# Optimization experiments

Measured on AMD Instinct MI355X. Metric: run time of the kernel, lower is better.

## Reference

```python
import jax, jax.numpy as jnp
import numpy as np

S, B, D, H, A = 256, 1024, 64, 128, 8  # seq_len, buffer, state_size, hidden, action_size


def _init(key, shape, fan_in):
    bound = 1.0 / np.sqrt(fan_in)
    return jax.random.uniform(key, shape, jnp.float32, -bound, bound)


def setup_inputs() -> dict:
    key = jax.random.key(0)
    ks = jax.random.split(key, 24)
    inp = {"state": jax.random.normal(ks[0], (S, B, D), jnp.float32)}
    # actor / critic MLPs (Linear(D,H) + ReLU + Linear(H,H) + ReLU)
    inp["aw1"] = _init(ks[1], (H, D), D); inp["ab1"] = _init(ks[2], (H,), D)
    inp["aw2"] = _init(ks[3], (H, H), H); inp["ab2"] = _init(ks[4], (H,), H)
    inp["cw1"] = _init(ks[5], (H, D), D); inp["cb1"] = _init(ks[6], (H,), D)
    inp["cw2"] = _init(ks[7], (H, H), H); inp["cb2"] = _init(ks[8], (H,), H)
    # LSTMs (PyTorch layout: W_ih [4H,H], W_hh [4H,H], gate order i,f,g,o)
    inp["a_wih"] = _init(ks[9], (4 * H, H), H); inp["a_whh"] = _init(ks[10], (4 * H, H), H)
    inp["a_bih"] = _init(ks[11], (4 * H,), H); inp["a_bhh"] = _init(ks[12], (4 * H,), H)
    inp["c_wih"] = _init(ks[13], (4 * H, H), H); inp["c_whh"] = _init(ks[14], (4 * H, H), H)
    inp["c_bih"] = _init(ks[15], (4 * H,), H); inp["c_bhh"] = _init(ks[16], (4 * H,), H)
    # heads
    inp["mw"] = _init(ks[17], (A, H), H); inp["mb"] = _init(ks[18], (A,), H)
    inp["lw"] = _init(ks[19], (A, H), H); inp["lb"] = _init(ks[20], (A,), H)
    inp["vw"] = _init(ks[21], (1, H), H); inp["vb"] = _init(ks[22], (1,), H)
    return inp


def _mlp(x, w1, b1, w2, b2):
    h = jax.nn.relu(jnp.einsum('sbd,hd->sbh', x, w1) + b1)
    return jax.nn.relu(jnp.einsum('sbh,gh->sbg', h, w2) + b2)


def _lstm_zero_state(x, w_ih, b_ih, b_hh):
    # Each timestep runs with fresh zero (h, c): the recurrent term vanishes,
    # so the whole sequence is one batched GEMM + gating (W_hh unused).
    gates = jnp.einsum('sbh,gh->sbg', x, w_ih) + b_ih + b_hh  # [S,B,4H]
    i, f, g, o = jnp.split(gates, 4, axis=-1)
    c = jax.nn.sigmoid(i) * jnp.tanh(g)  # f * c_prev = 0
    return jax.nn.sigmoid(o) * jnp.tanh(c)


def reference(state, aw1, ab1, aw2, ab2, cw1, cb1, cw2, cb2,
              a_wih, a_whh, a_bih, a_bhh, c_wih, c_whh, c_bih, c_bhh,
              mw, mb, lw, lb, vw, vb):
    actor_h = _lstm_zero_state(_mlp(state, aw1, ab1, aw2, ab2), a_wih, a_bih, a_bhh)
    critic_h = _lstm_zero_state(_mlp(state, cw1, cb1, cw2, cb2), c_wih, c_bih, c_bhh)
    mean = jnp.einsum('sbh,ah->sba', actor_h, mw) + mb
    std = jnp.exp(jnp.einsum('sbh,ah->sba', actor_h, lw) + lb)
    value = jnp.einsum('sbh,vh->sbv', critic_h, vw) + vb
    return (mean, std, value)
```

## Files before the change

### kernel.cpp

```cpp
#include <hip/hip_runtime.h>


#define NROWS (256 * 1024)
#define HID 128
#define ACTD 8

#define BARRIER_LDS() \
  asm volatile("s_waitcnt lgkmcnt(0)\ns_barrier" ::: "memory")

#define W1_OFF 0
#define W2_OFF 16384
#define WI_OFF 49152
#define WG_OFF 81920
#define WO_OFF 114688
#define PSTR 147456
#define HEAD_OFF (2 * PSTR)
#define GB_OFF (HEAD_OFF + 8192)

#define NEG_L (-1.4426950408889634f)
#define TWO_L (2.8853900817779268f)

typedef __attribute__((ext_vector_type(8))) short s16x8;
typedef __attribute__((ext_vector_type(4))) float fx4;
typedef __attribute__((ext_vector_type(2))) float fx2;
typedef __attribute__((ext_vector_type(2))) unsigned int u32x2;
typedef __attribute__((ext_vector_type(4))) unsigned int u32x4;

__device__ __forceinline__ unsigned int cvtpk(float lo, float hi) {
  unsigned int r;
  asm("v_cvt_pk_bf16_f32 %0, %1, %2" : "=v"(r) : "v"(lo), "v"(hi));
  return r;
}
__device__ __forceinline__ float ex2(float x) {
  return __builtin_amdgcn_exp2f(x);
}
__device__ __forceinline__ float frcp(float x) {
  return __builtin_amdgcn_rcpf(x);
}
__device__ __forceinline__ fx2 mk2(float a, float b) {
  fx2 v;
  v[0] = a;
  v[1] = b;
  return v;
}

__device__ __forceinline__ s16x8 frag_ld(const unsigned short* base, int row,
                                         int kbyte, int rowsh) {
  int byte = (row << rowsh) + (kbyte ^ ((row & 7) << 4));
  return *(const s16x8*)((const char*)base + byte);
}

struct wpair {
  s16x8 w0, w1;
};
template <int KC>
__device__ __forceinline__ wpair wload(const char* __restrict__ wimg, int wv,
                                       int kc, int woff) {
  wpair p;
  p.w0 = *(const s16x8*)(wimg + (((wv * 2 + 0) * KC + kc) << 10) + woff);
  p.w1 = *(const s16x8*)(wimg + (((wv * 2 + 1) * KC + kc) << 10) + woff);
  return p;
}

template <int ASH>
__device__ __forceinline__ void gemm_kc(const wpair& p,
                                        const unsigned short* at, int kbyte,
                                        int l15, fx4 acc[4][2]) {
#pragma unroll
  for (int jt = 0; jt < 4; ++jt) {
    s16x8 a = frag_ld(at, jt * 16 + l15, kbyte, ASH);
    acc[jt][0] = __builtin_amdgcn_mfma_f32_16x16x32_bf16(p.w0, a, acc[jt][0], 0, 0, 0);
    acc[jt][1] = __builtin_amdgcn_mfma_f32_16x16x32_bf16(p.w1, a, acc[jt][1], 0, 0, 0);
  }
}

__device__ __forceinline__ void zacc(fx4 acc[4][2]) {
#pragma unroll
  for (int j = 0; j < 4; ++j)
#pragma unroll
    for (int i = 0; i < 2; ++i) acc[j][i] = fx4{0.f, 0.f, 0.f, 0.f};
}
__device__ __forceinline__ void bacc(fx4 acc[4][2], const float* __restrict__ b,
                                     int fb, int g4) {
#pragma unroll
  for (int it = 0; it < 2; ++it) {
    fx4 bv = *(const fx4*)(b + fb + it * 16 + g4);
#pragma unroll
    for (int jt = 0; jt < 4; ++jt) acc[jt][it] = bv;
  }
}

__device__ __forceinline__ void epi_relu(fx4 acc[4][2], unsigned short* obuf,
                                         int fb, int lane) {
  const int g4 = (lane >> 4) << 2;
  const int l15 = lane & 15;
  char* ob = (char*)obuf;
#pragma unroll
  for (int it = 0; it < 2; ++it) {
    int n0 = fb + it * 16 + g4;
#pragma unroll
    for (int jt = 0; jt < 4; ++jt) {
      fx4 v = acc[jt][it];
#pragma unroll
      for (int r = 0; r < 4; ++r) v[r] = fmaxf(v[r], 0.0f);
      u32x2 u;
      u[0] = cvtpk(v[0], v[1]);
      u[1] = cvtpk(v[2], v[3]);
      int m = jt * 16 + l15;
      *(u32x2*)(ob + (m << 8) + ((n0 * 2) ^ ((m & 7) << 4))) = u;
    }
  }
}

__global__ void prep_weights(const float* __restrict__ aw1,
                             const float* __restrict__ aw2,
                             const float* __restrict__ awih,
                             const float* __restrict__ cw1,
                             const float* __restrict__ cw2,
                             const float* __restrict__ cwih,
                             const float* __restrict__ mw,
                             const float* __restrict__ lw,
                             const float* __restrict__ vw,
                             const float* __restrict__ abih,
                             const float* __restrict__ abhh,
                             const float* __restrict__ cbih,
                             const float* __restrict__ cbhh,
                             char* __restrict__ ws) {
  int y = blockIdx.y;
  int idx = blockIdx.x * 256 + threadIdx.x;
  if (y >= 12) {
    if (idx < 384) {
      float* dst = (float*)(ws + GB_OFF + (size_t)(y - 12) * 1536);
      const float* b0 = (y == 12) ? abih : cbih;
      const float* b1 = (y == 12) ? abhh : cbhh;
      int sect = idx >> 7, f = idx & 127;
      int srow = (sect == 0) ? f : (sect == 1) ? 256 + f : 384 + f;
      float scale = (sect == 1) ? TWO_L : NEG_L;
      dst[idx] = scale * (b0[srow] + b1[srow]);
    }
    return;
  }
  if (y >= 10) {
    if (idx >= 256) return;
    int row = idx >> 4, c16 = idx & 15, kc = c16 >> 2, ks = c16 & 3;
    fx4 v0 = {0.f, 0.f, 0.f, 0.f}, v1 = v0;
    if (y == 10) {
      const float* src = (row < 8) ? (mw + (size_t)row * HID + c16 * 8)
                                   : (lw + (size_t)(row - 8) * HID + c16 * 8);
      v0 = ((const fx4*)src)[0];
      v1 = ((const fx4*)src)[1];
    } else if (row == 0) {
      const float* src = vw + c16 * 8;
      v0 = ((const fx4*)src)[0];
      v1 = ((const fx4*)src)[1];
    }
    u32x4 u;
    u[0] = cvtpk(v0[0], v0[1]);
    u[1] = cvtpk(v0[2], v0[3]);
    u[2] = cvtpk(v1[0], v1[1]);
    u[3] = cvtpk(v1[2], v1[3]);
    int dst = ((kc * 4 + ks) * 16 + row) * 16;
    *(u32x4*)(ws + HEAD_OFF + (size_t)(y - 10) * 4096 + dst) = u;
    return;
  }
  const float* src;
  int nch, ksh, KC, off;
  switch (y) {
    case 0:  src = aw1;              nch = 1024; ksh = 3; KC = 2; off = W1_OFF;        break;
    case 1:  src = aw2;              nch = 2048; ksh = 4; KC = 4; off = W2_OFF;        break;
    case 2:  src = awih;             nch = 2048; ksh = 4; KC = 4; off = WI_OFF;        break;
    case 3:  src = awih + 256 * HID; nch = 2048; ksh = 4; KC = 4; off = WG_OFF;        break;
    case 4:  src = awih + 384 * HID; nch = 2048; ksh = 4; KC = 4; off = WO_OFF;        break;
    case 5:  src = cw1;              nch = 1024; ksh = 3; KC = 2; off = PSTR + W1_OFF; break;
    case 6:  src = cw2;              nch = 2048; ksh = 4; KC = 4; off = PSTR + W2_OFF; break;
    case 7:  src = cwih;             nch = 2048; ksh = 4; KC = 4; off = PSTR + WI_OFF; break;
    case 8:  src = cwih + 256 * HID; nch = 2048; ksh = 4; KC = 4; off = PSTR + WG_OFF; break;
    default: src = cwih + 384 * HID; nch = 2048; ksh = 4; KC = 4; off = PSTR + WO_OFF; break;
  }
  if (idx >= nch) return;
  int row = idx >> ksh;
  int c16 = idx & ((1 << ksh) - 1);
  int b2 = row >> 4, r = row & 15, kc = c16 >> 2, ks = c16 & 3;
  const fx4* gp = (const fx4*)(src + (size_t)idx * 8);
  fx4 v0 = gp[0], v1 = gp[1];
  u32x4 u;
  u[0] = cvtpk(v0[0], v0[1]);
  u[1] = cvtpk(v0[2], v0[3]);
  u[2] = cvtpk(v1[0], v1[1]);
  u[3] = cvtpk(v1[2], v1[3]);
  int dst = (((b2 * KC + kc) * 4 + ks) * 16 + r) * 16;
  *(u32x4*)(ws + off + dst) = u;
}

__global__ __launch_bounds__(256, 3) void fused_ac(
    const float* __restrict__ state, const float* __restrict__ ab1,
    const float* __restrict__ ab2, const float* __restrict__ cb1,
    const float* __restrict__ cb2, const float* __restrict__ mb,
    const float* __restrict__ lb, const float* __restrict__ vb,
    const char* __restrict__ ws, float* __restrict__ outp) {
  __shared__ __align__(16) unsigned short abuf[8192];
  __shared__ __align__(16) unsigned short hbuf[8192];

  const int tid = threadIdx.x;
  const int lane = tid & 63;
  const int wv = tid >> 6;
  const int l15 = lane & 15;
  const int g4 = (lane >> 4) << 2;
  const int kb0 = (lane >> 4) << 4;
  const int woff = ((lane >> 4) << 8) + (l15 << 4);
  const int fb = wv << 5;
  const int path = blockIdx.x >> 12;
  const int rbase = (blockIdx.x & 4095) << 6;

  const char* wsp = ws + (size_t)path * PSTR;
  const float* b1 = path ? cb1 : ab1;
  const float* b2 = path ? cb2 : ab2;
  const float* gb = (const float*)(ws + GB_OFF + (size_t)path * 1536);
  const char* himg = ws + HEAD_OFF + (size_t)path * 4096;

  float* meanp = outp;
  float* stdp = outp + (size_t)NROWS * ACTD;
  float* valp = outp + (size_t)NROWS * ACTD * 2;

  wpair w1a = wload<2>(wsp + W1_OFF, wv, 0, woff);
  wpair w1b = wload<2>(wsp + W1_OFF, wv, 1, woff);

  {
    const float* xg = state + (size_t)rbase * 64;
    char* ab = (char*)abuf;
#pragma unroll
    for (int i = 0; i < 2; ++i) {
      int idx = tid + i * 256;
      int r = idx >> 3, c = idx & 7;
      const fx4* gp = (const fx4*)(xg + idx * 8);
      fx4 v0 = gp[0], v1 = gp[1];
      u32x4 u;
      u[0] = cvtpk(v0[0], v0[1]);
      u[1] = cvtpk(v0[2], v0[3]);
      u[2] = cvtpk(v1[0], v1[1]);
      u[3] = cvtpk(v1[2], v1[3]);
      *(u32x4*)(ab + r * 128 + ((c << 4) ^ ((r & 7) << 4))) = u;
    }
  }
  BARRIER_LDS();

  fx4 acc[4][2];
  bacc(acc, b1, fb, g4);
  __builtin_amdgcn_s_setprio(1);
  gemm_kc<7>(w1a, abuf, 0 + kb0, l15, acc);
  gemm_kc<7>(w1b, abuf, 64 + kb0, l15, acc);
  __builtin_amdgcn_s_setprio(0);
  wpair w2a = wload<4>(wsp + W2_OFF, wv, 0, woff);
  wpair w2b = wload<4>(wsp + W2_OFF, wv, 1, woff);
  wpair w2c = wload<4>(wsp + W2_OFF, wv, 2, woff);
  wpair w2d = wload<4>(wsp + W2_OFF, wv, 3, woff);
  epi_relu(acc, hbuf, fb, lane);
  BARRIER_LDS();

  bacc(acc, b2, fb, g4);
  __builtin_amdgcn_s_setprio(1);
  gemm_kc<8>(w2a, hbuf, 0 + kb0, l15, acc);
  gemm_kc<8>(w2b, hbuf, 64 + kb0, l15, acc);
  gemm_kc<8>(w2c, hbuf, 128 + kb0, l15, acc);
  gemm_kc<8>(w2d, hbuf, 192 + kb0, l15, acc);
  __builtin_amdgcn_s_setprio(0);
  wpair pi0 = wload<4>(wsp + WI_OFF, wv, 0, woff);
  wpair pg0 = wload<4>(wsp + WG_OFF, wv, 0, woff);
  wpair po0 = wload<4>(wsp + WO_OFF, wv, 0, woff);
  epi_relu(acc, abuf, fb, lane);
  BARRIER_LDS();

  fx4 ai[4][2], ag[4][2], ao[4][2];
  zacc(ai);
  zacc(ag);
  zacc(ao);
  __builtin_amdgcn_s_setprio(1);
#pragma unroll
  for (int kc = 0; kc < 4; ++kc) {
    wpair pi = (kc == 0) ? pi0 : wload<4>(wsp + WI_OFF, wv, kc, woff);
    wpair pg = (kc == 0) ? pg0 : wload<4>(wsp + WG_OFF, wv, kc, woff);
    wpair po = (kc == 0) ? po0 : wload<4>(wsp + WO_OFF, wv, kc, woff);
    int kbyte = kc * 64 + kb0;
#pragma unroll
    for (int jt = 0; jt < 4; ++jt) {
      s16x8 a = frag_ld(abuf, jt * 16 + l15, kbyte, 8);
      ai[jt][0] = __builtin_amdgcn_mfma_f32_16x16x32_bf16(pi.w0, a, ai[jt][0], 0, 0, 0);
      ai[jt][1] = __builtin_amdgcn_mfma_f32_16x16x32_bf16(pi.w1, a, ai[jt][1], 0, 0, 0);
      ag[jt][0] = __builtin_amdgcn_mfma_f32_16x16x32_bf16(pg.w0, a, ag[jt][0], 0, 0, 0);
      ag[jt][1] = __builtin_amdgcn_mfma_f32_16x16x32_bf16(pg.w1, a, ag[jt][1], 0, 0, 0);
      ao[jt][0] = __builtin_amdgcn_mfma_f32_16x16x32_bf16(po.w0, a, ao[jt][0], 0, 0, 0);
      ao[jt][1] = __builtin_amdgcn_mfma_f32_16x16x32_bf16(po.w1, a, ao[jt][1], 0, 0, 0);
    }
  }
  __builtin_amdgcn_s_setprio(0);
  s16x8 hw0 = *(const s16x8*)(himg + (0 << 10) + woff);
  s16x8 hw1 = *(const s16x8*)(himg + (1 << 10) + woff);
  s16x8 hw2 = *(const s16x8*)(himg + (2 << 10) + woff);
  s16x8 hw3 = *(const s16x8*)(himg + (3 << 10) + woff);

  {
    char* ob = (char*)hbuf;
#pragma unroll
    for (int it = 0; it < 2; ++it) {
      fx4 pvi = *(const fx4*)(gb + fb + it * 16 + g4);
      fx4 pvg = *(const fx4*)(gb + 128 + fb + it * 16 + g4);
      fx4 pvo = *(const fx4*)(gb + 256 + fb + it * 16 + g4);
      int n0 = fb + it * 16 + g4;
#pragma unroll
      for (int jt = 0; jt < 4; ++jt) {
        u32x2 u;
#pragma unroll
        for (int p = 0; p < 2; ++p) {
          const int r0 = 2 * p, r1 = 2 * p + 1;
          fx2 vi = mk2(ai[jt][it][r0], ai[jt][it][r1]);
          fx2 vg = mk2(ag[jt][it][r0], ag[jt][it][r1]);
          fx2 vo = mk2(ao[jt][it][r0], ao[jt][it][r1]);
          fx2 ti = vi * NEG_L + mk2(pvi[r0], pvi[r1]);
          fx2 tg = vg * TWO_L + mk2(pvg[r0], pvg[r1]);
          fx2 to = vo * NEG_L + mk2(pvo[r0], pvo[r1]);
          fx2 Ei = mk2(ex2(ti[0]), ex2(ti[1]));
          fx2 Eg = mk2(ex2(tg[0]), ex2(tg[1]));
          fx2 Eo = mk2(ex2(to[0]), ex2(to[1]));
          fx2 d1 = (Eg + 1.0f) * (Ei + 1.0f);
          fx2 r1v = mk2(frcp(d1[0]), frcp(d1[1]));
          fx2 c = (Eg - 1.0f) * r1v;
          fx2 ea = c * TWO_L;
          fx2 Ec = mk2(ex2(ea[0]), ex2(ea[1]));
          fx2 d2 = (Ec + 1.0f) * (Eo + 1.0f);
          fx2 r2v = mk2(frcp(d2[0]), frcp(d2[1]));
          fx2 h2 = (Ec - 1.0f) * r2v;
          u[p] = cvtpk(h2[0], h2[1]);
        }
        int m = jt * 16 + l15;
        *(u32x2*)(ob + (m << 8) + ((n0 * 2) ^ ((m & 7) << 4))) = u;
      }
    }
  }
  BARRIER_LDS();

  fx4 ha = fx4{0.f, 0.f, 0.f, 0.f};
  __builtin_amdgcn_s_setprio(1);
  ha = __builtin_amdgcn_mfma_f32_16x16x32_bf16(
      hw0, frag_ld(hbuf, (wv << 4) + l15, 0 + kb0, 8), ha, 0, 0, 0);
  ha = __builtin_amdgcn_mfma_f32_16x16x32_bf16(
      hw1, frag_ld(hbuf, (wv << 4) + l15, 64 + kb0, 8), ha, 0, 0, 0);
  ha = __builtin_amdgcn_mfma_f32_16x16x32_bf16(
      hw2, frag_ld(hbuf, (wv << 4) + l15, 128 + kb0, 8), ha, 0, 0, 0);
  ha = __builtin_amdgcn_mfma_f32_16x16x32_bf16(
      hw3, frag_ld(hbuf, (wv << 4) + l15, 192 + kb0, 8), ha, 0, 0, 0);
  __builtin_amdgcn_s_setprio(0);

  int m = rbase + (wv << 4) + l15;
  if (path == 0) {
    if (g4 < 8) {
      fx4 v = ha + *(const fx4*)(mb + g4);
      *(fx4*)(meanp + (size_t)m * ACTD + g4) = v;
    } else {
      fx4 v;
#pragma unroll
      for (int r = 0; r < 4; ++r) v[r] = __expf(ha[r] + lb[g4 - 8 + r]);
      *(fx4*)(stdp + (size_t)m * ACTD + (g4 - 8)) = v;
    }
  } else if (g4 == 0) {
    valp[m] = ha[0] + vb[0];
  }
}

extern "C" void kernel_launch(void* const* d_in, const int* in_sizes, int n_in,
                              void* d_out, int out_size, void* d_ws,
                              size_t ws_size, hipStream_t stream) {
  (void)in_sizes; (void)n_in; (void)ws_size; (void)out_size;
  const float* state = (const float*)d_in[0];
  const float* aw1 = (const float*)d_in[1];
  const float* ab1 = (const float*)d_in[2];
  const float* aw2 = (const float*)d_in[3];
  const float* ab2 = (const float*)d_in[4];
  const float* cw1 = (const float*)d_in[5];
  const float* cb1 = (const float*)d_in[6];
  const float* cw2 = (const float*)d_in[7];
  const float* cb2 = (const float*)d_in[8];
  const float* awih = (const float*)d_in[9];
  const float* abih = (const float*)d_in[11];
  const float* abhh = (const float*)d_in[12];
  const float* cwih = (const float*)d_in[13];
  const float* cbih = (const float*)d_in[15];
  const float* cbhh = (const float*)d_in[16];
  const float* mw = (const float*)d_in[17];
  const float* mb = (const float*)d_in[18];
  const float* lw = (const float*)d_in[19];
  const float* lb = (const float*)d_in[20];
  const float* vw = (const float*)d_in[21];
  const float* vb = (const float*)d_in[22];
  char* ws = (char*)d_ws;

  prep_weights<<<dim3(8, 14), 256, 0, stream>>>(
      aw1, aw2, awih, cw1, cw2, cwih, mw, lw, vw, abih, abhh, cbih, cbhh, ws);
  fused_ac<<<8192, 256, 0, stream>>>(state, ab1, ab2, cb1, cb2, mb, lb, vb, ws,
                                     (float*)d_out);
}
```

Before: 117.4 us.

## Split LSTM gate GEMM into two row halves to raise occupancy to four blocks

The LSTM gate GEMM and its gating epilogue now run in two 32-row halves, each holding only half the i/g/o accumulators. Weight fragment prefetches are moved to the point of use rather than held ahead in registers. Together this cuts register pressure so launch bounds can rise from 3 to 4 blocks per CU, trading more weight reloads from global/L2 and less latency hiding inside each wave for more waves in flight.

Measured after the change: 154.4 us. 31.5% more time.

```diff
diff --git a/kernel.cpp b/kernel.cpp
--- a/kernel.cpp
+++ b/kernel.cpp
@@ -74,9 +74,9 @@
   }
 }
 
-__device__ __forceinline__ void zacc(fx4 acc[4][2]) {
-#pragma unroll
-  for (int j = 0; j < 4; ++j)
+__device__ __forceinline__ void zacc2(fx4 acc[2][2]) {
+#pragma unroll
+  for (int j = 0; j < 2; ++j)
 #pragma unroll
     for (int i = 0; i < 2; ++i) acc[j][i] = fx4{0.f, 0.f, 0.f, 0.f};
 }
@@ -192,7 +192,7 @@
   *(u32x4*)(ws + off + dst) = u;
 }
 
-__global__ __launch_bounds__(256, 3) void fused_ac(
+__global__ __launch_bounds__(256, 4) void fused_ac(
     const float* __restrict__ state, const float* __restrict__ ab1,
     const float* __restrict__ ab2, const float* __restrict__ cb1,
     const float* __restrict__ cb2, const float* __restrict__ mb,
@@ -252,8 +252,6 @@
   __builtin_amdgcn_s_setprio(0);
   wpair w2a = wload<4>(wsp + W2_OFF, wv, 0, woff);
   wpair w2b = wload<4>(wsp + W2_OFF, wv, 1, woff);
-  wpair w2c = wload<4>(wsp + W2_OFF, wv, 2, woff);
-  wpair w2d = wload<4>(wsp + W2_OFF, wv, 3, woff);
   epi_relu(acc, hbuf, fb, lane);
   BARRIER_LDS();
 
@@ -261,44 +259,44 @@
   __builtin_amdgcn_s_setprio(1);
   gemm_kc<8>(w2a, hbuf, 0 + kb0, l15, acc);
   gemm_kc<8>(w2b, hbuf, 64 + kb0, l15, acc);
-  gemm_kc<8>(w2c, hbuf, 128 + kb0, l15, acc);
-  gemm_kc<8>(w2d, hbuf, 192 + kb0, l15, acc);
+  {
+    wpair p = wload<4>(wsp + W2_OFF, wv, 2, woff);
+    gemm_kc<8>(p, hbuf, 128 + kb0, l15, acc);
+  }
+  {
+    wpair p = wload<4>(wsp + W2_OFF, wv, 3, woff);
+    gemm_kc<8>(p, hbuf, 192 + kb0, l15, acc);
+  }
   __builtin_amdgcn_s_setprio(0);
-  wpair pi0 = wload<4>(wsp + WI_OFF, wv, 0, woff);
-  wpair pg0 = wload<4>(wsp + WG_OFF, wv, 0, woff);
-  wpair po0 = wload<4>(wsp + WO_OFF, wv, 0, woff);
   epi_relu(acc, abuf, fb, lane);
   BARRIER_LDS();
 
-  fx4 ai[4][2], ag[4][2], ao[4][2];
-  zacc(ai);
-  zacc(ag);
-  zacc(ao);
-  __builtin_amdgcn_s_setprio(1);
-#pragma unroll
-  for (int kc = 0; kc < 4; ++kc) {
-    wpair pi = (kc == 0) ? pi0 : wload<4>(wsp + WI_OFF, wv, kc, woff);
-    wpair pg = (kc == 0) ? pg0 : wload<4>(wsp + WG_OFF, wv, kc, woff);
-    wpair po = (kc == 0) ? po0 : wload<4>(wsp + WO_OFF, wv, kc, woff);
-    int kbyte = kc * 64 + kb0;
-#pragma unroll
-    for (int jt = 0; jt < 4; ++jt) {
-      s16x8 a = frag_ld(abuf, jt * 16 + l15, kbyte, 8);
-      ai[jt][0] = __builtin_amdgcn_mfma_f32_16x16x32_bf16(pi.w0, a, ai[jt][0], 0, 0, 0);
-      ai[jt][1] = __builtin_amdgcn_mfma_f32_16x16x32_bf16(pi.w1, a, ai[jt][1], 0, 0, 0);
-      ag[jt][0] = __builtin_amdgcn_mfma_f32_16x16x32_bf16(pg.w0, a, ag[jt][0], 0, 0, 0);
-      ag[jt][1] = __builtin_amdgcn_mfma_f32_16x16x32_bf16(pg.w1, a, ag[jt][1], 0, 0, 0);
-      ao[jt][0] = __builtin_amdgcn_mfma_f32_16x16x32_bf16(po.w0, a, ao[jt][0], 0, 0, 0);
-      ao[jt][1] = __builtin_amdgcn_mfma_f32_16x16x32_bf16(po.w1, a, ao[jt][1], 0, 0, 0);
-    }
-  }
-  __builtin_amdgcn_s_setprio(0);
-  s16x8 hw0 = *(const s16x8*)(himg + (0 << 10) + woff);
-  s16x8 hw1 = *(const s16x8*)(himg + (1 << 10) + woff);
-  s16x8 hw2 = *(const s16x8*)(himg + (2 << 10) + woff);
-  s16x8 hw3 = *(const s16x8*)(himg + (3 << 10) + woff);
-
-  {
+#pragma unroll
+  for (int half = 0; half < 2; ++half) {
+    const int ro = half << 5;
+    fx4 ai[2][2], ag[2][2], ao[2][2];
+    zacc2(ai);
+    zacc2(ag);
+    zacc2(ao);
+    __builtin_amdgcn_s_setprio(1);
+#pragma unroll
+    for (int kc = 0; kc < 4; ++kc) {
+      wpair pi = wload<4>(wsp + WI_OFF, wv, kc, woff);
+      wpair pg = wload<4>(wsp + WG_OFF, wv, kc, woff);
+      wpair po = wload<4>(wsp + WO_OFF, wv, kc, woff);
+      int kbyte = kc * 64 + kb0;
+#pragma unroll
+      for (int jt = 0; jt < 2; ++jt) {
+        s16x8 a = frag_ld(abuf, ro + jt * 16 + l15, kbyte, 8);
+        ai[jt][0] = __builtin_amdgcn_mfma_f32_16x16x32_bf16(pi.w0, a, ai[jt][0], 0, 0, 0);
+        ai[jt][1] = __builtin_amdgcn_mfma_f32_16x16x32_bf16(pi.w1, a, ai[jt][1], 0, 0, 0);
+        ag[jt][0] = __builtin_amdgcn_mfma_f32_16x16x32_bf16(pg.w0, a, ag[jt][0], 0, 0, 0);
+        ag[jt][1] = __builtin_amdgcn_mfma_f32_16x16x32_bf16(pg.w1, a, ag[jt][1], 0, 0, 0);
+        ao[jt][0] = __builtin_amdgcn_mfma_f32_16x16x32_bf16(po.w0, a, ao[jt][0], 0, 0, 0);
+        ao[jt][1] = __builtin_amdgcn_mfma_f32_16x16x32_bf16(po.w1, a, ao[jt][1], 0, 0, 0);
+      }
+    }
+    __builtin_amdgcn_s_setprio(0);
     char* ob = (char*)hbuf;
 #pragma unroll
     for (int it = 0; it < 2; ++it) {
@@ -307,7 +305,7 @@
       fx4 pvo = *(const fx4*)(gb + 256 + fb + it * 16 + g4);
       int n0 = fb + it * 16 + g4;
 #pragma unroll
-      for (int jt = 0; jt < 4; ++jt) {
+      for (int jt = 0; jt < 2; ++jt) {
         u32x2 u;
 #pragma unroll
         for (int p = 0; p < 2; ++p) {
@@ -331,11 +329,15 @@
           fx2 h2 = (Ec - 1.0f) * r2v;
           u[p] = cvtpk(h2[0], h2[1]);
         }
-        int m = jt * 16 + l15;
+        int m = ro + jt * 16 + l15;
         *(u32x2*)(ob + (m << 8) + ((n0 * 2) ^ ((m & 7) << 4))) = u;
       }
     }
   }
+  s16x8 hw0 = *(const s16x8*)(himg + (0 << 10) + woff);
+  s16x8 hw1 = *(const s16x8*)(himg + (1 << 10) + woff);
+  s16x8 hw2 = *(const s16x8*)(himg + (2 << 10) + woff);
+  s16x8 hw3 = *(const s16x8*)(himg + (3 << 10) + woff);
   BARRIER_LDS();
 
   fx4 ha = fx4{0.f, 0.f, 0.f, 0.f};
```
